# Optimization experiments

Measured on AMD Instinct MI355X. Metric: run time of the kernel, lower is better.

The kernel has to match this reference:

```python
import jax, jax.numpy as jnp
import numpy as np

B, H, W, C = 4, 64, 64, 512
DQK = C // 8


def setup_inputs() -> dict:
    key = jax.random.key(0)
    k1, k2, k3, k4 = jax.random.split(key, 4)
    x = jax.random.normal(k1, (B, H, W, C), dtype=jnp.float32)
    kernel_f = jax.random.normal(k2, (1, 1, C, DQK), dtype=jnp.float32) * 0.02
    kernel_g = jax.random.normal(k3, (1, 1, C, DQK), dtype=jnp.float32) * 0.02
    kernel_h = jax.random.normal(k4, (1, 1, C, C), dtype=jnp.float32) * 0.02
    gamma = jnp.ones((1,), dtype=jnp.float32)  # nonzero so attention branch contributes
    return {"x": x, "kernel_f": kernel_f, "kernel_g": kernel_g,
            "kernel_h": kernel_h, "gamma": gamma}


def reference(x, kernel_f, kernel_g, kernel_h, gamma):
    b, h, w, c = x.shape
    n = h * w
    xt = x.reshape(b, n, c)  # 1x1 conv == per-pixel matmul
    f = jnp.einsum('bnc,cd->bnd', xt, kernel_f[0, 0])       # [b,n,dqk]
    g = jnp.einsum('bnc,cd->bnd', xt, kernel_g[0, 0])       # [b,n,dqk]
    v = jnp.einsum('bnc,cd->bnd', xt, kernel_h[0, 0])       # [b,n,c]
    s = jnp.einsum('bid,bjd->bij', f, g)                    # [b,n,n] = f @ g^T
    beta = jax.nn.softmax(s, axis=-1)
    out = jnp.einsum('bij,bjc->bic', beta, v)               # [b,n,c]
    out = out.reshape(b, h, w, c)
    return gamma * out + x
```

## Files before the change

kernel.cpp:

```cpp
#include <hip/hip_runtime.h>


typedef __bf16 bf16x8 __attribute__((ext_vector_type(8)));
typedef __bf16 bf16x2 __attribute__((ext_vector_type(2)));
typedef float f32x4 __attribute__((ext_vector_type(4)));
typedef unsigned int u32x4 __attribute__((ext_vector_type(4)));
typedef unsigned int u32;

#define L2E 1.4426950408889634f

__device__ __forceinline__ unsigned short f2bf(float f) {
    unsigned int u = __builtin_bit_cast(unsigned int, f);
    u += 0x7fffu + ((u >> 16) & 1u);
    return (unsigned short)(u >> 16);
}
__device__ __forceinline__ u32 cvtpk(float a, float b) {
    bf16x2 t; t[0] = (__bf16)a; t[1] = (__bf16)b;
    return __builtin_bit_cast(u32, t);
}
__device__ __forceinline__ bf16x8 ld8(const void* p) {
    u32x4 u = *reinterpret_cast<const u32x4*>(p);
    return __builtin_bit_cast(bf16x8, u);
}
__device__ __forceinline__ bf16x8 ldx(const float* p) {
    float4 a = *reinterpret_cast<const float4*>(p);
    float4 b = *reinterpret_cast<const float4*>(p + 4);
    u32x4 r;
    r.x = cvtpk(a.x, a.y); r.y = cvtpk(a.z, a.w);
    r.z = cvtpk(b.x, b.y); r.w = cvtpk(b.z, b.w);
    return __builtin_bit_cast(bf16x8, r);
}
__device__ __forceinline__ f32x4 mfma16(bf16x8 a, bf16x8 b, f32x4 c) {
    return __builtin_amdgcn_mfma_f32_16x16x32_bf16(a, b, c, 0, 0, 0);
}
__device__ __forceinline__ void gl2lds16(const void* g, void* l) {
    __builtin_amdgcn_global_load_lds(
        (const __attribute__((address_space(1))) u32*)g,
        (__attribute__((address_space(3))) u32*)l, 16, 0, 0);
}

__global__ __launch_bounds__(256) void cvt_w_all(const float* __restrict__ kf,
                                                 const float* __restrict__ kg,
                                                 const float* __restrict__ kh,
                                                 unsigned short* __restrict__ wst) {
    int idx = blockIdx.x * 256 + threadIdx.x;
    int j = idx & 7;
    int gi = idx >> 3;
    int c = gi % 640;
    int sq = gi / 640;
    int k = (sq >> 2) * 32 + (sq & 3) * 8 + j;
    float v;
    if (c < 64)       v = kf[k * 64 + c] * L2E;
    else if (c < 128) v = kg[k * 64 + (c - 64)];
    else              v = kh[k * 512 + (c - 128)];
    wst[idx] = f2bf(v);
}

__global__ __launch_bounds__(256, 2) void proj_k(const float* __restrict__ x,
                                                 const unsigned short* __restrict__ wst,
                                                 unsigned short* __restrict__ fq,
                                                 unsigned short* __restrict__ kst,
                                                 unsigned short* __restrict__ vst) {
    __shared__ __align__(16) unsigned char Wl[2][20480];
    __shared__ unsigned short Tl[64][72];

    int m0 = blockIdx.x * 64;
    int grp = blockIdx.y;
    int tid = threadIdx.x;
    int w = tid >> 6, l = tid & 63, g = l >> 4, i = l & 15;

    const char* wsrc = (const char*)wst + (size_t)w * 10240 + (size_t)grp * 5120 + l * 16;

#pragma unroll
    for (int s5 = 0; s5 < 5; s5++)
        gl2lds16(wsrc + s5 * 1024, &Wl[0][w * 5120 + s5 * 1024]);

    const float* xrow = x + (size_t)(m0 + 16 * w + i) * 512 + g * 8;
    bf16x8 af[16];
#pragma unroll
    for (int k = 0; k < 16; k++) af[k] = ldx(xrow + 32 * k);

    f32x4 acc[5][4];
#pragma unroll
    for (int t = 0; t < 5; t++)
#pragma unroll
        for (int cf = 0; cf < 4; cf++) acc[t][cf] = f32x4{0, 0, 0, 0};

    int rdoff = g * 5120 + i * 16;

#pragma unroll
    for (int q = 0; q < 16; q++) {
        __syncthreads();
        if (q < 15) {
            const char* src = wsrc + (size_t)(q + 1) * 40960;
#pragma unroll
            for (int s5 = 0; s5 < 5; s5++)
                gl2lds16(src + s5 * 1024, &Wl[(q + 1) & 1][w * 5120 + s5 * 1024]);
        }
        const unsigned char* Wb = &Wl[q & 1][0];
        __builtin_amdgcn_s_setprio(1);
#pragma unroll
        for (int t = 0; t < 5; t++)
#pragma unroll
            for (int cf = 0; cf < 4; cf++) {
                bf16x8 bb = ld8(Wb + rdoff + (t * 64 + 16 * cf) * 16);
                acc[t][cf] = mfma16(af[q], bb, acc[t][cf]);
            }
        __builtin_amdgcn_s_setprio(0);
    }

    int batch = m0 >> 12;
    int kt = (m0 & 4095) >> 6;
    unsigned short* kbase = kst + (size_t)batch * 262144 + (size_t)kt * 4096;
    unsigned short* vbase = vst + (size_t)batch * 2097152 + (size_t)kt * 32768;

#pragma unroll
    for (int t = 0; t < 5; t++) {
        if (grp == 0 && t == 0) {
#pragma unroll
            for (int cf = 0; cf < 4; cf++)
#pragma unroll
                for (int r = 0; r < 4; r++)
                    fq[(size_t)(m0 + 16 * w + 4 * g + r) * 64 + 16 * cf + i] =
                        f2bf(acc[t][cf][r]);
        } else {
            __syncthreads();
#pragma unroll
            for (int cf = 0; cf < 4; cf++) {
                ushort4 v4;
                v4.x = f2bf(acc[t][cf][0]); v4.y = f2bf(acc[t][cf][1]);
                v4.z = f2bf(acc[t][cf][2]); v4.w = f2bf(acc[t][cf][3]);
                *reinterpret_cast<ushort4*>(&Tl[16 * cf + i][16 * w + 4 * g]) = v4;
            }
            __syncthreads();
            if (grp == 0 && t == 1) {
#pragma unroll
                for (int ch = tid; ch < 512; ch += 256) {
                    int jf2 = ch >> 7, ks = (ch >> 6) & 1, l2 = ch & 63;
                    int g2 = l2 >> 4, i2 = l2 & 15;
                    ushort4 o0, o1;
                    o0.x = Tl[ks * 32 + 8 * g2 + 0][16 * jf2 + i2];
                    o0.y = Tl[ks * 32 + 8 * g2 + 1][16 * jf2 + i2];
                    o0.z = Tl[ks * 32 + 8 * g2 + 2][16 * jf2 + i2];
                    o0.w = Tl[ks * 32 + 8 * g2 + 3][16 * jf2 + i2];
                    o1.x = Tl[ks * 32 + 8 * g2 + 4][16 * jf2 + i2];
                    o1.y = Tl[ks * 32 + 8 * g2 + 5][16 * jf2 + i2];
                    o1.z = Tl[ks * 32 + 8 * g2 + 6][16 * jf2 + i2];
                    o1.w = Tl[ks * 32 + 8 * g2 + 7][16 * jf2 + i2];
                    unsigned short* dst = kbase + (size_t)(jf2 * 1024 + ks * 512 + l2 * 8);
                    *reinterpret_cast<ushort4*>(dst)     = o0;
                    *reinterpret_cast<ushort4*>(dst + 4) = o1;
                }
            } else {
                int n0 = (grp == 0) ? (t - 2) * 64 : 192 + t * 64;
#pragma unroll
                for (int ch = tid; ch < 512; ch += 256) {
                    int cc = ch >> 7, ks = (ch >> 6) & 1, l2 = ch & 63;
                    int g2 = l2 >> 4, i2 = l2 & 15;
                    int row = cc * 16 + i2;
                    int jb = 32 * ks + 4 * g2;
                    ushort4 o0, o1;
                    o0.x = Tl[row][jb + 0];  o0.y = Tl[row][jb + 1];
                    o0.z = Tl[row][jb + 2];  o0.w = Tl[row][jb + 3];
                    o1.x = Tl[row][jb + 16]; o1.y = Tl[row][jb + 17];
                    o1.z = Tl[row][jb + 18]; o1.w = Tl[row][jb + 19];
                    int c16 = (n0 >> 4) + cc;
                    unsigned short* dst = vbase + (size_t)(c16 * 1024 + ks * 512 + l2 * 8);
                    *reinterpret_cast<ushort4*>(dst)     = o0;
                    *reinterpret_cast<ushort4*>(dst + 4) = o1;
                }
            }
        }
    }
}

__global__ __launch_bounds__(1024, 4) void attn_k(const unsigned short* __restrict__ fq,
                                                  const unsigned short* __restrict__ kst,
                                                  const unsigned short* __restrict__ vst,
                                                  const float* __restrict__ x,
                                                  const float* __restrict__ gamma,
                                                  float* __restrict__ out) {
    __shared__ __align__(16) unsigned char Pl[2][8192];
    __shared__ float l_lds[64];

    int bid = blockIdx.x;
    int xcd = bid & 7;
    int batch = xcd >> 1;
    int qidx = ((xcd & 1) << 5) | (bid >> 3);
    int q0 = qidx * 64;

    int tid = threadIdx.x;
    int w = tid >> 6, l = tid & 63, g = l >> 4, i = l & 15;
    int qf_s = w >> 2, jf = w & 3;

    if (tid < 64) l_lds[tid] = 0.0f;

    const unsigned short* fqb = fq + (size_t)batch * 4096 * 64;
    const char* kb = (const char*)kst + (size_t)batch * 524288;
    const char* vb = (const char*)vst + (size_t)batch * 4194304;

    bf16x8 aQ[2];
#pragma unroll
    for (int ks = 0; ks < 2; ks++)
        aQ[ks] = ld8(fqb + (size_t)(q0 + 16 * qf_s + i) * 64 + ks * 32 + g * 8);

    f32x4 acc[4][2];
#pragma unroll
    for (int a = 0; a < 4; a++)
#pragma unroll
        for (int b = 0; b < 2; b++) acc[a][b] = f32x4{0, 0, 0, 0};
    float lp = 0.0f;

    int pwoff = (qf_s * 2 + (jf >> 1)) * 1024 + l * 16 + (jf & 1) * 8;
    int c16w = w * 2;

    bf16x8 kA[2];
    kA[0] = ld8(kb + (size_t)jf * 2048 + l * 16);
    kA[1] = ld8(kb + (size_t)jf * 2048 + 1024 + l * 16);

    bf16x8 vbr[2][2][2];
#pragma unroll
    for (int cf = 0; cf < 2; cf++)
#pragma unroll
        for (int ks = 0; ks < 2; ks++)
            vbr[0][cf][ks] = ld8(vb + (size_t)(c16w + cf) * 2048 + ks * 1024 + l * 16);

    {
        f32x4 sacc = f32x4{0, 0, 0, 0};
        sacc = mfma16(kA[0], aQ[0], sacc);
        sacc = mfma16(kA[1], aQ[1], sacc);
        kA[0] = ld8(kb + (size_t)(4 + jf) * 2048 + l * 16);
        kA[1] = ld8(kb + (size_t)(4 + jf) * 2048 + 1024 + l * 16);
        float p0 = __builtin_amdgcn_exp2f(sacc[0]);
        float p1 = __builtin_amdgcn_exp2f(sacc[1]);
        float p2 = __builtin_amdgcn_exp2f(sacc[2]);
        float p3 = __builtin_amdgcn_exp2f(sacc[3]);
        lp += (p0 + p1) + (p2 + p3);
        uint2 pk2;
        pk2.x = cvtpk(p0, p1);
        pk2.y = cvtpk(p2, p3);
        *reinterpret_cast<uint2*>(&Pl[0][0] + pwoff) = pk2;
    }

#pragma unroll 2
    for (int t = 0; t < 64; ++t) {
        asm volatile("s_waitcnt lgkmcnt(0)" ::: "memory");
        __builtin_amdgcn_s_barrier();

        f32x4 sacc = f32x4{0, 0, 0, 0};
        sacc = mfma16(kA[0], aQ[0], sacc);
        sacc = mfma16(kA[1], aQ[1], sacc);

        {
            int tk = (t + 2) & 63;
            const char* kn = kb + (size_t)(tk * 4 + jf) * 2048;
            kA[0] = ld8(kn + l * 16);
            kA[1] = ld8(kn + 1024 + l * 16);
        }

        {
            int tv = (t + 1) & 63;
#pragma unroll
            for (int cf = 0; cf < 2; cf++)
#pragma unroll
                for (int ks = 0; ks < 2; ks++)
                    vbr[(t + 1) & 1][cf][ks] =
                        ld8(vb + (size_t)(tv * 32 + c16w + cf) * 2048 + ks * 1024 + l * 16);
        }

        const unsigned char* Pr = &Pl[t & 1][0];
        __builtin_amdgcn_s_setprio(1);
#pragma unroll
        for (int qf = 0; qf < 4; qf++) {
            bf16x8 aP0 = ld8(Pr + (qf * 2 + 0) * 1024 + l * 16);
            bf16x8 aP1 = ld8(Pr + (qf * 2 + 1) * 1024 + l * 16);
#pragma unroll
            for (int cf = 0; cf < 2; cf++) {
                acc[qf][cf] = mfma16(aP0, vbr[t & 1][cf][0], acc[qf][cf]);
                acc[qf][cf] = mfma16(aP1, vbr[t & 1][cf][1], acc[qf][cf]);
            }
        }
        __builtin_amdgcn_s_setprio(0);

        float msk = (t < 63) ? 1.0f : 0.0f;
        unsigned char* Pb = &Pl[(t + 1) & 1][0];
        {
            float p0 = __builtin_amdgcn_exp2f(sacc[0]);
            float p1 = __builtin_amdgcn_exp2f(sacc[1]);
            float p2 = __builtin_amdgcn_exp2f(sacc[2]);
            float p3 = __builtin_amdgcn_exp2f(sacc[3]);
            lp += msk * ((p0 + p1) + (p2 + p3));
            uint2 pk2;
            pk2.x = cvtpk(p0, p1);
            pk2.y = cvtpk(p2, p3);
            *reinterpret_cast<uint2*>(Pb + pwoff) = pk2;
        }
    }

    lp += __shfl_xor(lp, 16, 64);
    lp += __shfl_xor(lp, 32, 64);
    if (g == 0) atomicAdd(&l_lds[16 * qf_s + i], lp);
    __syncthreads();

    float gam = gamma[0];
#pragma unroll
    for (int qf = 0; qf < 4; qf++) {
#pragma unroll
        for (int r = 0; r < 4; r++) {
            float linv = gam / l_lds[16 * qf + 4 * g + r];
            int n = q0 + 16 * qf + 4 * g + r;
            size_t base = ((size_t)batch * 4096 + n) * 512 + 32 * w;
#pragma unroll
            for (int cf = 0; cf < 2; cf++)
                out[base + 16 * cf + i] = acc[qf][cf][r] * linv + x[base + 16 * cf + i];
        }
    }
}


extern "C" void kernel_launch(void* const* d_in, const int* in_sizes, int n_in,
                              void* d_out, int out_size, void* d_ws, size_t ws_size,
                              hipStream_t stream) {
    const float* x = (const float*)d_in[0];
    const float* kf = (const float*)d_in[1];
    const float* kg = (const float*)d_in[2];
    const float* kh = (const float*)d_in[3];
    const float* gamma = (const float*)d_in[4];
    float* out = (float*)d_out;

    char* ws = (char*)d_ws;
    unsigned short* Fq  = (unsigned short*)(ws);
    unsigned short* Kst = (unsigned short*)(ws + 2097152);
    unsigned short* Vst = (unsigned short*)(ws + 4194304);
    unsigned short* Wst = (unsigned short*)(ws + 20971520);

    cvt_w_all<<<1280, 256, 0, stream>>>(kf, kg, kh, Wst);
    proj_k<<<dim3(256, 2), 256, 0, stream>>>(x, Wst, Fq, Kst, Vst);
    attn_k<<<256, 1024, 0, stream>>>(Fq, Kst, Vst, x, gamma, out);
}
```

Baseline: 113.9 us.

## Process two key tiles per barrier in the attention loop

The main attention loop now handles two 64-key tiles per iteration, using four P buffers in shared memory and two sets of K/V register fragments. This halves the number of workgroup barriers and lgkmcnt waits across the 64 tiles. The price is more VGPRs (extra K and V fragments plus a second score accumulator) and double the P shared memory, which may hurt occupancy under the 1024x4 launch bounds.

```diff
diff --git a/kernel.cpp b/kernel.cpp
--- a/kernel.cpp
+++ b/kernel.cpp
@@ -180,7 +180,7 @@
                                                   const float* __restrict__ x,
                                                   const float* __restrict__ gamma,
                                                   float* __restrict__ out) {
-    __shared__ __align__(16) unsigned char Pl[2][8192];
+    __shared__ __align__(16) unsigned char Pl[4][8192];
     __shared__ float l_lds[64];
 
     int bid = blockIdx.x;
@@ -214,86 +214,129 @@
     int pwoff = (qf_s * 2 + (jf >> 1)) * 1024 + l * 16 + (jf & 1) * 8;
     int c16w = w * 2;
 
-    bf16x8 kA[2];
-    kA[0] = ld8(kb + (size_t)jf * 2048 + l * 16);
-    kA[1] = ld8(kb + (size_t)jf * 2048 + 1024 + l * 16);
-
-    bf16x8 vbr[2][2][2];
+    bf16x8 kAa[2], kAb[2];
+    kAa[0] = ld8(kb + (size_t)jf * 2048 + l * 16);
+    kAa[1] = ld8(kb + (size_t)jf * 2048 + 1024 + l * 16);
+    kAb[0] = ld8(kb + (size_t)(4 + jf) * 2048 + l * 16);
+    kAb[1] = ld8(kb + (size_t)(4 + jf) * 2048 + 1024 + l * 16);
+
+    bf16x8 vbr_a[2][2], vbr_b[2][2];
 #pragma unroll
     for (int cf = 0; cf < 2; cf++)
 #pragma unroll
-        for (int ks = 0; ks < 2; ks++)
-            vbr[0][cf][ks] = ld8(vb + (size_t)(c16w + cf) * 2048 + ks * 1024 + l * 16);
+        for (int ks = 0; ks < 2; ks++) {
+            vbr_a[cf][ks] = ld8(vb + (size_t)(c16w + cf) * 2048 + ks * 1024 + l * 16);
+            vbr_b[cf][ks] = ld8(vb + (size_t)(32 + c16w + cf) * 2048 + ks * 1024 + l * 16);
+        }
 
     {
-        f32x4 sacc = f32x4{0, 0, 0, 0};
-        sacc = mfma16(kA[0], aQ[0], sacc);
-        sacc = mfma16(kA[1], aQ[1], sacc);
-        kA[0] = ld8(kb + (size_t)(4 + jf) * 2048 + l * 16);
-        kA[1] = ld8(kb + (size_t)(4 + jf) * 2048 + 1024 + l * 16);
-        float p0 = __builtin_amdgcn_exp2f(sacc[0]);
-        float p1 = __builtin_amdgcn_exp2f(sacc[1]);
-        float p2 = __builtin_amdgcn_exp2f(sacc[2]);
-        float p3 = __builtin_amdgcn_exp2f(sacc[3]);
+        f32x4 s0 = f32x4{0,0,0,0}, s1 = f32x4{0,0,0,0};
+        s0 = mfma16(kAa[0], aQ[0], s0); s0 = mfma16(kAa[1], aQ[1], s0);
+        s1 = mfma16(kAb[0], aQ[0], s1); s1 = mfma16(kAb[1], aQ[1], s1);
+        kAa[0] = ld8(kb + (size_t)(8 + jf) * 2048 + l * 16);
+        kAa[1] = ld8(kb + (size_t)(8 + jf) * 2048 + 1024 + l * 16);
+        kAb[0] = ld8(kb + (size_t)(12 + jf) * 2048 + l * 16);
+        kAb[1] = ld8(kb + (size_t)(12 + jf) * 2048 + 1024 + l * 16);
+        float p0 = __builtin_amdgcn_exp2f(s0[0]);
+        float p1 = __builtin_amdgcn_exp2f(s0[1]);
+        float p2 = __builtin_amdgcn_exp2f(s0[2]);
+        float p3 = __builtin_amdgcn_exp2f(s0[3]);
         lp += (p0 + p1) + (p2 + p3);
-        uint2 pk2;
-        pk2.x = cvtpk(p0, p1);
-        pk2.y = cvtpk(p2, p3);
+        uint2 pk2; pk2.x = cvtpk(p0, p1); pk2.y = cvtpk(p2, p3);
         *reinterpret_cast<uint2*>(&Pl[0][0] + pwoff) = pk2;
+        p0 = __builtin_amdgcn_exp2f(s1[0]);
+        p1 = __builtin_amdgcn_exp2f(s1[1]);
+        p2 = __builtin_amdgcn_exp2f(s1[2]);
+        p3 = __builtin_amdgcn_exp2f(s1[3]);
+        lp += (p0 + p1) + (p2 + p3);
+        pk2.x = cvtpk(p0, p1); pk2.y = cvtpk(p2, p3);
+        *reinterpret_cast<uint2*>(&Pl[1][0] + pwoff) = pk2;
     }
 
 #pragma unroll 2
-    for (int t = 0; t < 64; ++t) {
+    for (int u = 0; u < 32; ++u) {
         asm volatile("s_waitcnt lgkmcnt(0)" ::: "memory");
         __builtin_amdgcn_s_barrier();
 
-        f32x4 sacc = f32x4{0, 0, 0, 0};
-        sacc = mfma16(kA[0], aQ[0], sacc);
-        sacc = mfma16(kA[1], aQ[1], sacc);
+        const unsigned char* Pr0 = &Pl[(u & 1) * 2][0];
+        const unsigned char* Pr1 = Pr0 + 8192;
+
+        f32x4 s0 = f32x4{0,0,0,0}, s1 = f32x4{0,0,0,0};
+        s0 = mfma16(kAa[0], aQ[0], s0); s0 = mfma16(kAa[1], aQ[1], s0);
+        s1 = mfma16(kAb[0], aQ[0], s1); s1 = mfma16(kAb[1], aQ[1], s1);
 
         {
-            int tk = (t + 2) & 63;
-            const char* kn = kb + (size_t)(tk * 4 + jf) * 2048;
-            kA[0] = ld8(kn + l * 16);
-            kA[1] = ld8(kn + 1024 + l * 16);
-        }
-
+            int ta = (2 * u + 4) & 63, tb = (2 * u + 5) & 63;
+            const char* ka = kb + (size_t)(ta * 4 + jf) * 2048;
+            const char* kp = kb + (size_t)(tb * 4 + jf) * 2048;
+            kAa[0] = ld8(ka + l * 16);
+            kAa[1] = ld8(ka + 1024 + l * 16);
+            kAb[0] = ld8(kp + l * 16);
+            kAb[1] = ld8(kp + 1024 + l * 16);
+        }
+
+        __builtin_amdgcn_s_setprio(1);
+#pragma unroll
+        for (int qf = 0; qf < 4; qf++) {
+            bf16x8 aP0 = ld8(Pr0 + (qf * 2 + 0) * 1024 + l * 16);
+            bf16x8 aP1 = ld8(Pr0 + (qf * 2 + 1) * 1024 + l * 16);
+#pragma unroll
+            for (int cf = 0; cf < 2; cf++) {
+                acc[qf][cf] = mfma16(aP0, vbr_a[cf][0], acc[qf][cf]);
+                acc[qf][cf] = mfma16(aP1, vbr_a[cf][1], acc[qf][cf]);
+            }
+        }
+        __builtin_amdgcn_s_setprio(0);
         {
-            int tv = (t + 1) & 63;
+            int tv = (2 * u + 2) & 63;
 #pragma unroll
             for (int cf = 0; cf < 2; cf++)
 #pragma unroll
                 for (int ks = 0; ks < 2; ks++)
-                    vbr[(t + 1) & 1][cf][ks] =
-                        ld8(vb + (size_t)(tv * 32 + c16w + cf) * 2048 + ks * 1024 + l * 16);
-        }
-
-        const unsigned char* Pr = &Pl[t & 1][0];
+                    vbr_a[cf][ks] = ld8(vb + (size_t)(tv * 32 + c16w + cf) * 2048 +
+                                        ks * 1024 + l * 16);
+        }
+
         __builtin_amdgcn_s_setprio(1);
 #pragma unroll
         for (int qf = 0; qf < 4; qf++) {
-            bf16x8 aP0 = ld8(Pr + (qf * 2 + 0) * 1024 + l * 16);
-            bf16x8 aP1 = ld8(Pr + (qf * 2 + 1) * 1024 + l * 16);
+            bf16x8 aP0 = ld8(Pr1 + (qf * 2 + 0) * 1024 + l * 16);
+            bf16x8 aP1 = ld8(Pr1 + (qf * 2 + 1) * 1024 + l * 16);
 #pragma unroll
             for (int cf = 0; cf < 2; cf++) {
-                acc[qf][cf] = mfma16(aP0, vbr[t & 1][cf][0], acc[qf][cf]);
-                acc[qf][cf] = mfma16(aP1, vbr[t & 1][cf][1], acc[qf][cf]);
+                acc[qf][cf] = mfma16(aP0, vbr_b[cf][0], acc[qf][cf]);
+                acc[qf][cf] = mfma16(aP1, vbr_b[cf][1], acc[qf][cf]);
             }
         }
         __builtin_amdgcn_s_setprio(0);
-
-        float msk = (t < 63) ? 1.0f : 0.0f;
-        unsigned char* Pb = &Pl[(t + 1) & 1][0];
         {
-            float p0 = __builtin_amdgcn_exp2f(sacc[0]);
-            float p1 = __builtin_amdgcn_exp2f(sacc[1]);
-            float p2 = __builtin_amdgcn_exp2f(sacc[2]);
-            float p3 = __builtin_amdgcn_exp2f(sacc[3]);
+            int tv = (2 * u + 3) & 63;
+#pragma unroll
+            for (int cf = 0; cf < 2; cf++)
+#pragma unroll
+                for (int ks = 0; ks < 2; ks++)
+                    vbr_b[cf][ks] = ld8(vb + (size_t)(tv * 32 + c16w + cf) * 2048 +
+                                        ks * 1024 + l * 16);
+        }
+
+        float msk = (u < 31) ? 1.0f : 0.0f;
+        unsigned char* Pw0 = &Pl[((u + 1) & 1) * 2][0];
+        unsigned char* Pw1 = Pw0 + 8192;
+        {
+            float p0 = __builtin_amdgcn_exp2f(s0[0]);
+            float p1 = __builtin_amdgcn_exp2f(s0[1]);
+            float p2 = __builtin_amdgcn_exp2f(s0[2]);
+            float p3 = __builtin_amdgcn_exp2f(s0[3]);
             lp += msk * ((p0 + p1) + (p2 + p3));
-            uint2 pk2;
-            pk2.x = cvtpk(p0, p1);
-            pk2.y = cvtpk(p2, p3);
-            *reinterpret_cast<uint2*>(Pb + pwoff) = pk2;
+            uint2 pk2; pk2.x = cvtpk(p0, p1); pk2.y = cvtpk(p2, p3);
+            *reinterpret_cast<uint2*>(Pw0 + pwoff) = pk2;
+            p0 = __builtin_amdgcn_exp2f(s1[0]);
+            p1 = __builtin_amdgcn_exp2f(s1[1]);
+            p2 = __builtin_amdgcn_exp2f(s1[2]);
+            p3 = __builtin_amdgcn_exp2f(s1[3]);
+            lp += msk * ((p0 + p1) + (p2 + p3));
+            pk2.x = cvtpk(p0, p1); pk2.y = cvtpk(p2, p3);
+            *reinterpret_cast<uint2*>(Pw1 + pwoff) = pk2;
         }
     }
 
```

Result: slower. 132.2 us (+16.1%).
